# Performance work log

Measured on AMD Instinct MI355X. Metric: run time of the kernel, lower is better.

## Reference

```python
import jax, jax.numpy as jnp
import numpy as np

K_NEIGHBOURS = 16
ITERATIONS = 3
NUM_CLASSES = 20
N_POINTS = 20000


def setup_inputs() -> dict:
    key = jax.random.key(0)
    k1, k2 = jax.random.split(key)
    logits = jax.random.normal(k1, (N_POINTS, NUM_CLASSES), dtype=jnp.float32)
    coords = jax.random.uniform(k2, (N_POINTS, 3), dtype=jnp.float32)
    # nn.init.eye_ then *= -0.1
    compat_w = (-0.1 * jnp.eye(NUM_CLASSES, dtype=jnp.float32))
    return {"logits": logits, "coords": coords, "compat_w": compat_w}


def _knn_graph(coords, k):
    # torch.cdist (p=2): euclidean distances, (N, N)
    sq = jnp.sum(coords * coords, axis=-1)
    d2 = sq[:, None] + sq[None, :] - 2.0 * (coords @ coords.T)
    dists = jnp.sqrt(jnp.clip(d2, 0.0))
    # smallest-k -> top_k of negated distances
    _, idx = jax.lax.top_k(-dists, k)  # (N, k)
    return idx


def reference(logits, coords, compat_w):
    knn_idx = _knn_graph(coords, K_NEIGHBOURS)
    q = jax.nn.softmax(logits, axis=-1)
    for _ in range(ITERATIONS):
        neighbour_q = q[knn_idx]            # (N, k, K) gather
        msg = jnp.mean(neighbour_q, axis=1)  # (N, K)
        refined = logits + msg @ compat_w.T  # nn.Linear: x @ W^T
        q = jax.nn.softmax(refined, axis=-1)
    return (refined, q)
```

## Files before the change

### kernel.cpp

```cpp
#include <hip/hip_runtime.h>

#define N_PTS 20000
#define NCLS 20
#define KNN 16
#define GRID 12
#define NCELLS (GRID * GRID * GRID)
#define HCELL (1.0f / (float)GRID)
#define CAND_CAP 640
#define KEY_CAP 128
#define R_TARGET 0.0680f

__device__ __forceinline__ int cell1d(float v) {
    int c = (int)(v * (float)GRID);
    return min(max(c, 0), GRID - 1);
}

__global__ __launch_bounds__(256) void count_scan_kernel(const float* __restrict__ coords,
                                                         int* __restrict__ cellCount,
                                                         int* __restrict__ doneCtr,
                                                         int* __restrict__ cellStart,
                                                         int* __restrict__ cellCursor) {
    const int p = blockIdx.x * blockDim.x + threadIdx.x;
    if (p < N_PTS) {
        const int cx = cell1d(coords[3 * p + 0]);
        const int cy = cell1d(coords[3 * p + 1]);
        const int cz = cell1d(coords[3 * p + 2]);
        atomicAdd(&cellCount[(cz * GRID + cy) * GRID + cx], 1);
    }
    __syncthreads();
    __shared__ bool isLast;
    if (threadIdx.x == 0)
        isLast = (atomicAdd(doneCtr, 1) == (int)gridDim.x - 1);
    __syncthreads();
    if (!isLast) return;

    __shared__ int part[256];
    const int t = threadIdx.x;
    const int base = t * 7;
    int local[7];
    int s = 0;
#pragma unroll
    for (int i = 0; i < 7; ++i) {
        const int c = base + i;
        const int v = (c < NCELLS)
            ? __hip_atomic_load(&cellCount[c], __ATOMIC_RELAXED, __HIP_MEMORY_SCOPE_AGENT)
            : 0;
        local[i] = s;
        s += v;
    }
    part[t] = s;
    __syncthreads();
    for (int off = 1; off < 256; off <<= 1) {
        const int v = part[t] + ((t >= off) ? part[t - off] : 0);
        __syncthreads();
        part[t] = v;
        __syncthreads();
    }
    const int excl = (t > 0) ? part[t - 1] : 0;
#pragma unroll
    for (int i = 0; i < 7; ++i) {
        const int c = base + i;
        if (c < NCELLS) {
            cellStart[c] = excl + local[i];
            cellCursor[c] = excl + local[i];
        }
    }
    if (t == 255) cellStart[NCELLS] = part[255];
}

__global__ __launch_bounds__(256) void scatter_kernel(const float* __restrict__ coords,
                                                      const float* __restrict__ logits,
                                                      int* __restrict__ cellCursor,
                                                      float4* __restrict__ sortedPts,
                                                      int* __restrict__ orig,
                                                      float* __restrict__ ls,
                                                      float* __restrict__ q0s) {
    const int p = blockIdx.x * blockDim.x + threadIdx.x;
    if (p >= N_PTS) return;
    const float x = coords[3 * p + 0];
    const float y = coords[3 * p + 1];
    const float z = coords[3 * p + 2];
    const int c = (cell1d(z) * GRID + cell1d(y)) * GRID + cell1d(x);
    const int pos = atomicAdd(&cellCursor[c], 1);
    sortedPts[pos] = make_float4(x, y, z, __uint_as_float((unsigned)p));
    orig[pos] = p;
    const float4* l4 = (const float4*)(logits + p * NCLS);
    float v[NCLS];
#pragma unroll
    for (int u = 0; u < 5; ++u) {
        const float4 a = l4[u];
        v[4 * u + 0] = a.x; v[4 * u + 1] = a.y;
        v[4 * u + 2] = a.z; v[4 * u + 3] = a.w;
    }
    float4* d4 = (float4*)(ls + pos * NCLS);
#pragma unroll
    for (int u = 0; u < 5; ++u)
        d4[u] = make_float4(v[4 * u], v[4 * u + 1], v[4 * u + 2], v[4 * u + 3]);
    float mx = v[0];
#pragma unroll
    for (int cc = 1; cc < NCLS; ++cc) mx = fmaxf(mx, v[cc]);
    float sum = 0.f;
#pragma unroll
    for (int cc = 0; cc < NCLS; ++cc) { v[cc] = __expf(v[cc] - mx); sum += v[cc]; }
    const float inv = 1.f / sum;
    float4* q4 = (float4*)(q0s + pos * NCLS);
#pragma unroll
    for (int u = 0; u < 5; ++u)
        q4[u] = make_float4(v[4 * u] * inv, v[4 * u + 1] * inv,
                            v[4 * u + 2] * inv, v[4 * u + 3] * inv);
}

__device__ void knn_ladder(const float4* __restrict__ sortedPts,
                           const int* __restrict__ cellStart,
                           const float4 qp, const int s, int hw,
                           unsigned long long* keys, const int lane,
                           int* __restrict__ knn_out) {
    const unsigned long long laneLt = (1ull << lane) - 1ull;
    const int cx = cell1d(qp.x), cy = cell1d(qp.y), cz = cell1d(qp.z);
    float g = 0.9995f * (float)hw * HCELL;
    float tau = g * g;
    int cnt = 0;
    for (int att = 0; att < 16; ++att) {
        cnt = 0;
        const int xlo = max(cx - hw, 0), xhi = min(cx + hw, GRID - 1);
        const int ylo = max(cy - hw, 0), yhi = min(cy + hw, GRID - 1);
        const int zlo = max(cz - hw, 0), zhi = min(cz + hw, GRID - 1);
        for (int zz = zlo; zz <= zhi; ++zz) {
            for (int yy = ylo; yy <= yhi; ++yy) {
                const int rowc = (zz * GRID + yy) * GRID;
                const int beg = cellStart[rowc + xlo];
                const int end = cellStart[rowc + xhi + 1];
                for (int j0 = beg; j0 < end; j0 += 64) {
                    const int j = j0 + lane;
                    const bool jv = j < end;
                    const float4 pt = sortedPts[jv ? j : beg];
                    const float dx = pt.x - qp.x, dy = pt.y - qp.y, dz = pt.z - qp.z;
                    const float d2 = dx * dx + dy * dy + dz * dz;
                    const bool take = jv && (d2 < tau);
                    const unsigned long long mm = __ballot(take);
                    if (take) {
                        const int pos = cnt + (int)__popcll(mm & laneLt);
                        if (pos < KEY_CAP)
                            keys[pos] = (((unsigned long long)__float_as_uint(d2)) << 32) |
                                        (unsigned long long)(unsigned)j;
                    }
                    cnt += (int)__popcll(mm);
                }
            }
        }
        if (cnt >= KNN && cnt <= KEY_CAP) break;
        if (cnt < KNN) {
            if (hw < GRID - 1) { ++hw; g = 0.9995f * (float)hw * HCELL; tau = g * g; }
            else tau *= 2.5f;
        } else {
            tau *= 0.6f;
        }
    }
    const int m = min(cnt, KEY_CAP);
    const unsigned long long k0 = (lane < m) ? keys[lane] : ~0ull;
    const unsigned long long k1 = (lane + 64 < m) ? keys[lane + 64] : ~0ull;
    int r0 = 0, r1 = 0;
    for (int j = 0; j < m; ++j) {
        const unsigned long long kj = keys[j];
        r0 += (kj < k0); r1 += (kj < k1);
    }
    if (lane < m && r0 < KNN)      knn_out[s * KNN + r0] = (int)(unsigned)(k0 & 0xffffffffull);
    if (lane + 64 < m && r1 < KNN) knn_out[s * KNN + r1] = (int)(unsigned)(k1 & 0xffffffffull);
}

__global__ __launch_bounds__(256) void knn_kernel(const float4* __restrict__ sortedPts,
                                                  const int* __restrict__ cellStart,
                                                  int* __restrict__ knn_out) {
    __shared__ float4 cand[CAND_CAP];
    __shared__ unsigned long long keys[4][KEY_CAP];
    const int lane = threadIdx.x & 63;
    const int wave = threadIdx.x >> 6;
    const int c = blockIdx.x;
    const int cz = c / (GRID * GRID);
    const int cy = (c / GRID) % GRID;
    const int cx = c % GRID;
    const int pbeg = cellStart[c];
    const int pend = cellStart[c + 1];
    const int npts = pend - pbeg;
    if (npts <= 0) return;
    const int bd = (cx == 0 || cx == GRID - 1) + (cy == 0 || cy == GRID - 1) +
                   (cz == 0 || cz == GRID - 1);
    const int hs = (bd >= 2) ? 2 : 1;
    const unsigned long long laneLt = (1ull << lane) - 1ull;

    const int xlo = max(cx - hs, 0), xhi = min(cx + hs, GRID - 1);
    const int ylo = max(cy - hs, 0), yhi = min(cy + hs, GRID - 1);
    const int zlo = max(cz - hs, 0), zhi = min(cz + hs, GRID - 1);
    const int ny = yhi - ylo + 1;
    const int nruns = (zhi - zlo + 1) * ny;

    int beg = 0, len = 0;
    if (lane < nruns) {
        const int zz = zlo + lane / ny;
        const int yy = ylo + lane % ny;
        const int rowc = (zz * GRID + yy) * GRID;
        beg = cellStart[rowc + xlo];
        len = cellStart[rowc + xhi + 1] - beg;
    }
    int off = len;
#pragma unroll
    for (int sh = 1; sh < 32; sh <<= 1) {
        const int o = __shfl_up(off, sh, 64);
        if (lane >= sh) off += o;
    }
    const int nc = __shfl(off, nruns - 1);
    off -= len;
    const int ownRun = (cz - zlo) * ny + (cy - ylo);
    const int ownOff = __shfl(off, ownRun) + (pbeg - __shfl(beg, ownRun));

    if (nc <= CAND_CAP) {
        for (int r = wave; r < nruns; r += 4) {
            const int rb = __shfl(beg, r);
            const int rl = __shfl(len, r);
            const int ro = __shfl(off, r);
            for (int i = lane; i < rl; i += 64) {
                float4 pt = sortedPts[rb + i];
                pt.w = __uint_as_float((unsigned)(rb + i));
                cand[ro + i] = pt;
            }
        }
    }
    __syncthreads();

    if (nc > CAND_CAP) {
        for (int idx = wave; idx < npts; idx += 4)
            knn_ladder(sortedPts, cellStart, sortedPts[pbeg + idx], pbeg + idx,
                       hs, keys[wave], lane, knn_out);
        return;
    }

    const float taumaxr = 0.9995f * (float)hs * HCELL;
    const float taumax = taumaxr * taumaxr;

    for (int idx = wave; idx < npts; idx += 4) {
        const int s = pbeg + idx;
        const float4 qp = cand[ownOff + idx];
        float r = R_TARGET;
        const float inv2r = 0.5f / r;
        const float fx = (fminf(qp.x + r, 1.f) - fmaxf(qp.x - r, 0.f)) * inv2r;
        const float fy = (fminf(qp.y + r, 1.f) - fmaxf(qp.y - r, 0.f)) * inv2r;
        const float fz = (fminf(qp.z + r, 1.f) - fmaxf(qp.z - r, 0.f)) * inv2r;
        const float f = fmaxf(fx * fy * fz, 0.05f);
        r = R_TARGET * __powf(f, -0.33333334f);
        float tau = fminf(r * r, taumax);
        bool triedMax = (tau >= taumax * 0.999f);

        int cnt = 0;
        bool ok = false;
        for (int att = 0; att < 5 && !ok; ++att) {
            cnt = 0;
            for (int j0 = 0; j0 < nc; j0 += 64) {
                const int j = j0 + lane;
                float d2 = 1e30f;
                unsigned pw = 0;
                if (j < nc) {
                    const float4 pt = cand[j];
                    const float dx = pt.x - qp.x, dy = pt.y - qp.y, dz = pt.z - qp.z;
                    d2 = dx * dx + dy * dy + dz * dz;
                    pw = __float_as_uint(pt.w);
                }
                const bool take = d2 < tau;
                const unsigned long long mm = __ballot(take);
                if (take) {
                    const int pos = cnt + (int)__popcll(mm & laneLt);
                    if (pos < KEY_CAP)
                        keys[wave][pos] =
                            (((unsigned long long)__float_as_uint(d2)) << 32) |
                            (unsigned long long)pw;
                }
                cnt += (int)__popcll(mm);
            }
            if (cnt >= KNN && cnt <= KEY_CAP) ok = true;
            else if (cnt < KNN) {
                if (triedMax) break;
                tau = taumax; triedMax = true;
            } else tau *= 0.6f;
        }
        if (!ok) {
            knn_ladder(sortedPts, cellStart, qp, s, hs + 1, keys[wave], lane, knn_out);
            continue;
        }
        const int m = cnt;
        const unsigned long long k0 = (lane < m) ? keys[wave][lane] : ~0ull;
        const unsigned long long k1 = (lane + 64 < m) ? keys[wave][lane + 64] : ~0ull;
        int r0 = 0, r1 = 0;
        for (int j = 0; j < m; ++j) {
            const unsigned long long kj = keys[wave][j];
            r0 += (kj < k0); r1 += (kj < k1);
        }
        if (lane < m && r0 < KNN)      knn_out[s * KNN + r0] = (int)(unsigned)(k0 & 0xffffffffull);
        if (lane + 64 < m && r1 < KNN) knn_out[s * KNN + r1] = (int)(unsigned)(k1 & 0xffffffffull);
    }
}

__global__ __launch_bounds__(256) void crf_iter_kernel(const float* __restrict__ ls,
                                                       const float* __restrict__ W,
                                                       const int* __restrict__ knn,
                                                       const float* __restrict__ qin,
                                                       float* __restrict__ qout,
                                                       const int* __restrict__ orig,
                                                       float* __restrict__ outRef,
                                                       float* __restrict__ outQ) {
    __shared__ float Ws[NCLS * NCLS];
    for (int i = threadIdx.x; i < NCLS * NCLS; i += blockDim.x) Ws[i] = W[i];
    __syncthreads();
    const int t = blockIdx.x * blockDim.x + threadIdx.x;
    const int p = t >> 3;
    const int sub = t & 7;
    if (p >= N_PTS) return;

    float acc[NCLS];
#pragma unroll
    for (int c = 0; c < NCLS; ++c) acc[c] = 0.f;

    const int2 k2 = ((const int2*)(knn + p * KNN))[sub];
    const int ids[2] = {k2.x, k2.y};
#pragma unroll
    for (int u = 0; u < 2; ++u) {
        unsigned id = (unsigned)ids[u];
        if (id >= N_PTS) id = 0;
        const float4* r4 = (const float4*)(qin + id * NCLS);
#pragma unroll
        for (int v = 0; v < 5; ++v) {
            const float4 a = r4[v];
            acc[4 * v + 0] += a.x; acc[4 * v + 1] += a.y;
            acc[4 * v + 2] += a.z; acc[4 * v + 3] += a.w;
        }
    }
#pragma unroll
    for (int c = 0; c < NCLS; ++c) {
        acc[c] += __shfl_xor(acc[c], 1, 64);
        acc[c] += __shfl_xor(acc[c], 2, 64);
        acc[c] += __shfl_xor(acc[c], 4, 64);
        acc[c] *= (1.f / 16.f);
    }

    const int c0 = (sub & 3) * 5;
    float ref[5];
#pragma unroll
    for (int i = 0; i < 5; ++i) {
        float s = ls[p * NCLS + c0 + i];
#pragma unroll
        for (int k = 0; k < NCLS; ++k) s += acc[k] * Ws[(c0 + i) * NCLS + k];
        ref[i] = s;
    }

    float mx = ref[0];
#pragma unroll
    for (int i = 1; i < 5; ++i) mx = fmaxf(mx, ref[i]);
    mx = fmaxf(mx, __shfl_xor(mx, 1, 64));
    mx = fmaxf(mx, __shfl_xor(mx, 2, 64));
    float ex[5];
    float ps = 0.f;
#pragma unroll
    for (int i = 0; i < 5; ++i) { ex[i] = __expf(ref[i] - mx); ps += ex[i]; }
    ps += __shfl_xor(ps, 1, 64);
    ps += __shfl_xor(ps, 2, 64);
    const float inv = 1.f / ps;

    if (sub < 4) {
        if (outRef != nullptr) {
            const int o = orig[p];
#pragma unroll
            for (int i = 0; i < 5; ++i) {
                outRef[o * NCLS + c0 + i] = ref[i];
                outQ[o * NCLS + c0 + i] = ex[i] * inv;
            }
        } else {
#pragma unroll
            for (int i = 0; i < 5; ++i) qout[p * NCLS + c0 + i] = ex[i] * inv;
        }
    }
}

extern "C" void kernel_launch(void* const* d_in, const int* in_sizes, int n_in,
                              void* d_out, int out_size, void* d_ws, size_t ws_size,
                              hipStream_t stream) {
    const float* logits = (const float*)d_in[0];
    const float* coords = (const float*)d_in[1];
    const float* W      = (const float*)d_in[2];
    float* out = (float*)d_out;

    char* ws = (char*)d_ws;
    size_t off = 0;
    int* knn = (int*)(ws + off);              off += (size_t)N_PTS * KNN * 4;
    off = (off + 255) & ~(size_t)255;
    float* ls = (float*)(ws + off);           off += (size_t)N_PTS * NCLS * 4;
    off = (off + 255) & ~(size_t)255;
    float* q0s = (float*)(ws + off);          off += (size_t)N_PTS * NCLS * 4;
    off = (off + 255) & ~(size_t)255;
    float4* sortedPts = (float4*)(ws + off);  off += (size_t)N_PTS * 16;
    off = (off + 255) & ~(size_t)255;
    int* orig = (int*)(ws + off);             off += (size_t)N_PTS * 4;
    off = (off + 255) & ~(size_t)255;
    int* cellCount = (int*)(ws + off);        off += (size_t)(NCELLS + 1) * 4;
    int* doneCtr   = cellCount + NCELLS;
    off = (off + 255) & ~(size_t)255;
    int* cellStart = (int*)(ws + off);        off += (size_t)(NCELLS + 1) * 4;
    off = (off + 255) & ~(size_t)255;
    int* cellCursor = (int*)(ws + off);
    float* q1s = out + N_PTS * NCLS;

    const int threads = 256;
    const int pblocks = (N_PTS + threads - 1) / threads;
    const int cblocks = (8 * N_PTS + threads - 1) / threads;

    hipMemsetAsync(cellCount, 0, (NCELLS + 1) * sizeof(int), stream);
    count_scan_kernel<<<pblocks, threads, 0, stream>>>(coords, cellCount, doneCtr,
                                                       cellStart, cellCursor);
    scatter_kernel<<<pblocks, threads, 0, stream>>>(coords, logits, cellCursor,
                                                    sortedPts, orig, ls, q0s);
    knn_kernel<<<NCELLS, threads, 0, stream>>>(sortedPts, cellStart, knn);
    crf_iter_kernel<<<cblocks, threads, 0, stream>>>(ls, W, knn, q0s, q1s, orig,
                                                     nullptr, nullptr);
    crf_iter_kernel<<<cblocks, threads, 0, stream>>>(ls, W, knn, q1s, q0s, orig,
                                                     nullptr, nullptr);
    crf_iter_kernel<<<cblocks, threads, 0, stream>>>(ls, W, knn, q0s, nullptr, orig,
                                                     out, out + N_PTS * NCLS);
}
```

Baseline: 126.3 us.

## Fuse first CRF iteration into kNN kernel per grid cell

Merges the kNN search kernel with the first CRF message-passing iteration, so each cell block computes neighbour lists and then immediately gathers softmax probabilities for its own points and writes q1. This removes one kernel launch and lets the block read its just-written knn rows while they are likely still in cache. It also adds a launch_bounds occupancy hint of 8 and a shared copy of the compat matrix. In exchange, blocks with few points underuse lanes in the CRF phase, and register pressure from the fused code may reduce occupancy.

Result: slower. 152.8 us (+21.0%).

```diff
diff --git a/kernel.cpp b/kernel.cpp
--- a/kernel.cpp
+++ b/kernel.cpp
@@ -168,11 +168,16 @@
     if (lane + 64 < m && r1 < KNN) knn_out[s * KNN + r1] = (int)(unsigned)(k1 & 0xffffffffull);
 }
 
-__global__ __launch_bounds__(256) void knn_kernel(const float4* __restrict__ sortedPts,
-                                                  const int* __restrict__ cellStart,
-                                                  int* __restrict__ knn_out) {
+__global__ __launch_bounds__(256, 8) void knn_crf1_kernel(const float4* __restrict__ sortedPts,
+                                                          const int* __restrict__ cellStart,
+                                                          const float* __restrict__ ls,
+                                                          const float* __restrict__ W,
+                                                          const float* __restrict__ q0s,
+                                                          int* __restrict__ knn_out,
+                                                          float* __restrict__ q1s) {
     __shared__ float4 cand[CAND_CAP];
     __shared__ unsigned long long keys[4][KEY_CAP];
+    __shared__ float Ws[NCLS * NCLS];
     const int lane = threadIdx.x & 63;
     const int wave = threadIdx.x >> 6;
     const int c = blockIdx.x;
@@ -183,6 +188,7 @@
     const int pend = cellStart[c + 1];
     const int npts = pend - pbeg;
     if (npts <= 0) return;
+    for (int i = threadIdx.x; i < NCLS * NCLS; i += 256) Ws[i] = W[i];
     const int bd = (cx == 0 || cx == GRID - 1) + (cy == 0 || cy == GRID - 1) +
                    (cz == 0 || cz == GRID - 1);
     const int hs = (bd >= 2) ? 2 : 1;
@@ -231,70 +237,129 @@
         for (int idx = wave; idx < npts; idx += 4)
             knn_ladder(sortedPts, cellStart, sortedPts[pbeg + idx], pbeg + idx,
                        hs, keys[wave], lane, knn_out);
-        return;
-    }
-
-    const float taumaxr = 0.9995f * (float)hs * HCELL;
-    const float taumax = taumaxr * taumaxr;
-
-    for (int idx = wave; idx < npts; idx += 4) {
+    } else {
+        const float taumaxr = 0.9995f * (float)hs * HCELL;
+        const float taumax = taumaxr * taumaxr;
+
+        for (int idx = wave; idx < npts; idx += 4) {
+            const int s = pbeg + idx;
+            const float4 qp = cand[ownOff + idx];
+            float r = R_TARGET;
+            const float inv2r = 0.5f / r;
+            const float fx = (fminf(qp.x + r, 1.f) - fmaxf(qp.x - r, 0.f)) * inv2r;
+            const float fy = (fminf(qp.y + r, 1.f) - fmaxf(qp.y - r, 0.f)) * inv2r;
+            const float fz = (fminf(qp.z + r, 1.f) - fmaxf(qp.z - r, 0.f)) * inv2r;
+            const float f = fmaxf(fx * fy * fz, 0.05f);
+            r = R_TARGET * __powf(f, -0.33333334f);
+            float tau = fminf(r * r, taumax);
+            bool triedMax = (tau >= taumax * 0.999f);
+
+            int cnt = 0;
+            bool ok = false;
+            for (int att = 0; att < 5 && !ok; ++att) {
+                cnt = 0;
+                for (int j0 = 0; j0 < nc; j0 += 64) {
+                    const int j = j0 + lane;
+                    float d2 = 1e30f;
+                    unsigned pw = 0;
+                    if (j < nc) {
+                        const float4 pt = cand[j];
+                        const float dx = pt.x - qp.x, dy = pt.y - qp.y, dz = pt.z - qp.z;
+                        d2 = dx * dx + dy * dy + dz * dz;
+                        pw = __float_as_uint(pt.w);
+                    }
+                    const bool take = d2 < tau;
+                    const unsigned long long mm = __ballot(take);
+                    if (take) {
+                        const int pos = cnt + (int)__popcll(mm & laneLt);
+                        if (pos < KEY_CAP)
+                            keys[wave][pos] =
+                                (((unsigned long long)__float_as_uint(d2)) << 32) |
+                                (unsigned long long)pw;
+                    }
+                    cnt += (int)__popcll(mm);
+                }
+                if (cnt >= KNN && cnt <= KEY_CAP) ok = true;
+                else if (cnt < KNN) {
+                    if (triedMax) break;
+                    tau = taumax; triedMax = true;
+                } else tau *= 0.6f;
+            }
+            if (!ok) {
+                knn_ladder(sortedPts, cellStart, qp, s, hs + 1, keys[wave], lane, knn_out);
+                continue;
+            }
+            const int m = cnt;
+            const unsigned long long k0 = (lane < m) ? keys[wave][lane] : ~0ull;
+            const unsigned long long k1 = (lane + 64 < m) ? keys[wave][lane + 64] : ~0ull;
+            int r0 = 0, r1 = 0;
+            for (int j = 0; j < m; ++j) {
+                const unsigned long long kj = keys[wave][j];
+                r0 += (kj < k0); r1 += (kj < k1);
+            }
+            if (lane < m && r0 < KNN)
+                knn_out[s * KNN + r0] = (int)(unsigned)(k0 & 0xffffffffull);
+            if (lane + 64 < m && r1 < KNN)
+                knn_out[s * KNN + r1] = (int)(unsigned)(k1 & 0xffffffffull);
+        }
+    }
+    __syncthreads();
+
+    const int g = lane >> 2;
+    const int sub = lane & 3;
+    const int c0 = sub * 5;
+    for (int idx = wave * 16 + g; idx < npts; idx += 64) {
         const int s = pbeg + idx;
-        const float4 qp = cand[ownOff + idx];
-        float r = R_TARGET;
-        const float inv2r = 0.5f / r;
-        const float fx = (fminf(qp.x + r, 1.f) - fmaxf(qp.x - r, 0.f)) * inv2r;
-        const float fy = (fminf(qp.y + r, 1.f) - fmaxf(qp.y - r, 0.f)) * inv2r;
-        const float fz = (fminf(qp.z + r, 1.f) - fmaxf(qp.z - r, 0.f)) * inv2r;
-        const float f = fmaxf(fx * fy * fz, 0.05f);
-        r = R_TARGET * __powf(f, -0.33333334f);
-        float tau = fminf(r * r, taumax);
-        bool triedMax = (tau >= taumax * 0.999f);
-
-        int cnt = 0;
-        bool ok = false;
-        for (int att = 0; att < 5 && !ok; ++att) {
-            cnt = 0;
-            for (int j0 = 0; j0 < nc; j0 += 64) {
-                const int j = j0 + lane;
-                float d2 = 1e30f;
-                unsigned pw = 0;
-                if (j < nc) {
-                    const float4 pt = cand[j];
-                    const float dx = pt.x - qp.x, dy = pt.y - qp.y, dz = pt.z - qp.z;
-                    d2 = dx * dx + dy * dy + dz * dz;
-                    pw = __float_as_uint(pt.w);
+        const int4 k4 = ((const int4*)(knn_out + s * KNN))[sub];
+        float ref[5];
+#pragma unroll
+        for (int i = 0; i < 5; ++i) ref[i] = ls[s * NCLS + c0 + i];
+#pragma unroll
+        for (int half = 0; half < 2; ++half) {
+            float acc[10];
+#pragma unroll
+            for (int i = 0; i < 10; ++i) acc[i] = 0.f;
+            const int ids[4] = {k4.x, k4.y, k4.z, k4.w};
+#pragma unroll
+            for (int u = 0; u < 4; ++u) {
+                unsigned id = (unsigned)ids[u];
+                if (id >= N_PTS) id = 0;
+                const float2* r2 = (const float2*)(q0s + id * NCLS) + half * 5;
+#pragma unroll
+                for (int v = 0; v < 5; ++v) {
+                    const float2 a = r2[v];
+                    acc[2 * v + 0] += a.x;
+                    acc[2 * v + 1] += a.y;
                 }
-                const bool take = d2 < tau;
-                const unsigned long long mm = __ballot(take);
-                if (take) {
-                    const int pos = cnt + (int)__popcll(mm & laneLt);
-                    if (pos < KEY_CAP)
-                        keys[wave][pos] =
-                            (((unsigned long long)__float_as_uint(d2)) << 32) |
-                            (unsigned long long)pw;
-                }
-                cnt += (int)__popcll(mm);
-            }
-            if (cnt >= KNN && cnt <= KEY_CAP) ok = true;
-            else if (cnt < KNN) {
-                if (triedMax) break;
-                tau = taumax; triedMax = true;
-            } else tau *= 0.6f;
-        }
-        if (!ok) {
-            knn_ladder(sortedPts, cellStart, qp, s, hs + 1, keys[wave], lane, knn_out);
-            continue;
-        }
-        const int m = cnt;
-        const unsigned long long k0 = (lane < m) ? keys[wave][lane] : ~0ull;
-        const unsigned long long k1 = (lane + 64 < m) ? keys[wave][lane + 64] : ~0ull;
-        int r0 = 0, r1 = 0;
-        for (int j = 0; j < m; ++j) {
-            const unsigned long long kj = keys[wave][j];
-            r0 += (kj < k0); r1 += (kj < k1);
-        }
-        if (lane < m && r0 < KNN)      knn_out[s * KNN + r0] = (int)(unsigned)(k0 & 0xffffffffull);
-        if (lane + 64 < m && r1 < KNN) knn_out[s * KNN + r1] = (int)(unsigned)(k1 & 0xffffffffull);
+            }
+#pragma unroll
+            for (int k = 0; k < 10; ++k) {
+                acc[k] += __shfl_xor(acc[k], 1, 64);
+                acc[k] += __shfl_xor(acc[k], 2, 64);
+            }
+#pragma unroll
+            for (int i = 0; i < 5; ++i) {
+                float sv = 0.f;
+#pragma unroll
+                for (int k = 0; k < 10; ++k)
+                    sv += acc[k] * Ws[(c0 + i) * NCLS + half * 10 + k];
+                ref[i] += sv * (1.f / 16.f);
+            }
+        }
+        float mx = ref[0];
+#pragma unroll
+        for (int i = 1; i < 5; ++i) mx = fmaxf(mx, ref[i]);
+        mx = fmaxf(mx, __shfl_xor(mx, 1, 64));
+        mx = fmaxf(mx, __shfl_xor(mx, 2, 64));
+        float ex[5];
+        float ps = 0.f;
+#pragma unroll
+        for (int i = 0; i < 5; ++i) { ex[i] = __expf(ref[i] - mx); ps += ex[i]; }
+        ps += __shfl_xor(ps, 1, 64);
+        ps += __shfl_xor(ps, 2, 64);
+        const float inv = 1.f / ps;
+#pragma unroll
+        for (int i = 0; i < 5; ++i) q1s[s * NCLS + c0 + i] = ex[i] * inv;
     }
 }
 
@@ -415,9 +480,8 @@
                                                        cellStart, cellCursor);
     scatter_kernel<<<pblocks, threads, 0, stream>>>(coords, logits, cellCursor,
                                                     sortedPts, orig, ls, q0s);
-    knn_kernel<<<NCELLS, threads, 0, stream>>>(sortedPts, cellStart, knn);
-    crf_iter_kernel<<<cblocks, threads, 0, stream>>>(ls, W, knn, q0s, q1s, orig,
-                                                     nullptr, nullptr);
+    knn_crf1_kernel<<<NCELLS, threads, 0, stream>>>(sortedPts, cellStart, ls, W,
+                                                    q0s, knn, q1s);
     crf_iter_kernel<<<cblocks, threads, 0, stream>>>(ls, W, knn, q1s, q0s, orig,
                                                      nullptr, nullptr);
     crf_iter_kernel<<<cblocks, threads, 0, stream>>>(ls, W, knn, q0s, nullptr, orig,
```

## Fuse count/scan and scatter into one kernel with a spin-wait ready flag

Applied to the files above, without the earlier changes.

Merges the counting/prefix-scan kernel and the scatter kernel into a single build kernel. The last block to finish counting performs the scan and sets a global ready flag, while every block spins on that flag before scattering. This removes one kernel launch and the boundary between the two stages, and reuses coordinates already held in registers. In exchange it relies on all 79 blocks being co-resident, which they are on this GPU; otherwise the spin-wait could deadlock.

New measurement: 125.0 us. No clear change (-1.0%).

```diff
diff --git a/kernel.cpp b/kernel.cpp
--- a/kernel.cpp
+++ b/kernel.cpp
@@ -15,72 +15,79 @@
     return min(max(c, 0), GRID - 1);
 }
 
-__global__ __launch_bounds__(256) void count_scan_kernel(const float* __restrict__ coords,
-                                                         int* __restrict__ cellCount,
-                                                         int* __restrict__ doneCtr,
-                                                         int* __restrict__ cellStart,
-                                                         int* __restrict__ cellCursor) {
+__global__ __launch_bounds__(256) void build_kernel(const float* __restrict__ coords,
+                                                    const float* __restrict__ logits,
+                                                    int* __restrict__ cellCount,
+                                                    int* __restrict__ doneCtr,
+                                                    int* __restrict__ readyFlag,
+                                                    int* __restrict__ cellStart,
+                                                    int* __restrict__ cellCursor,
+                                                    float4* __restrict__ sortedPts,
+                                                    int* __restrict__ orig,
+                                                    float* __restrict__ ls,
+                                                    float* __restrict__ q0s) {
     const int p = blockIdx.x * blockDim.x + threadIdx.x;
-    if (p < N_PTS) {
-        const int cx = cell1d(coords[3 * p + 0]);
-        const int cy = cell1d(coords[3 * p + 1]);
-        const int cz = cell1d(coords[3 * p + 2]);
-        atomicAdd(&cellCount[(cz * GRID + cy) * GRID + cx], 1);
+    const bool act = (p < N_PTS);
+    float x = 0.f, y = 0.f, z = 0.f;
+    int c = 0;
+    if (act) {
+        x = coords[3 * p + 0];
+        y = coords[3 * p + 1];
+        z = coords[3 * p + 2];
+        c = (cell1d(z) * GRID + cell1d(y)) * GRID + cell1d(x);
+        atomicAdd(&cellCount[c], 1);
     }
     __syncthreads();
     __shared__ bool isLast;
     if (threadIdx.x == 0)
         isLast = (atomicAdd(doneCtr, 1) == (int)gridDim.x - 1);
     __syncthreads();
-    if (!isLast) return;
-
-    __shared__ int part[256];
-    const int t = threadIdx.x;
-    const int base = t * 7;
-    int local[7];
-    int s = 0;
-#pragma unroll
-    for (int i = 0; i < 7; ++i) {
-        const int c = base + i;
-        const int v = (c < NCELLS)
-            ? __hip_atomic_load(&cellCount[c], __ATOMIC_RELAXED, __HIP_MEMORY_SCOPE_AGENT)
-            : 0;
-        local[i] = s;
-        s += v;
-    }
-    part[t] = s;
+
+    if (isLast) {
+        __shared__ int part[256];
+        const int t = threadIdx.x;
+        const int base = t * 7;
+        int local[7];
+        int s = 0;
+#pragma unroll
+        for (int i = 0; i < 7; ++i) {
+            const int cc = base + i;
+            const int v = (cc < NCELLS)
+                ? __hip_atomic_load(&cellCount[cc], __ATOMIC_RELAXED, __HIP_MEMORY_SCOPE_AGENT)
+                : 0;
+            local[i] = s;
+            s += v;
+        }
+        part[t] = s;
+        __syncthreads();
+        for (int off2 = 1; off2 < 256; off2 <<= 1) {
+            const int v = part[t] + ((t >= off2) ? part[t - off2] : 0);
+            __syncthreads();
+            part[t] = v;
+            __syncthreads();
+        }
+        const int excl = (t > 0) ? part[t - 1] : 0;
+#pragma unroll
+        for (int i = 0; i < 7; ++i) {
+            const int cc = base + i;
+            if (cc < NCELLS) {
+                cellStart[cc] = excl + local[i];
+                __hip_atomic_store(&cellCursor[cc], excl + local[i],
+                                   __ATOMIC_RELAXED, __HIP_MEMORY_SCOPE_AGENT);
+            }
+        }
+        if (t == 255) cellStart[NCELLS] = part[255];
+        __syncthreads();
+        if (t == 0)
+            __hip_atomic_store(readyFlag, 1, __ATOMIC_RELAXED, __HIP_MEMORY_SCOPE_AGENT);
+    }
+    if (threadIdx.x == 0) {
+        while (__hip_atomic_load(readyFlag, __ATOMIC_RELAXED, __HIP_MEMORY_SCOPE_AGENT) == 0)
+            __builtin_amdgcn_s_sleep(2);
+    }
     __syncthreads();
-    for (int off = 1; off < 256; off <<= 1) {
-        const int v = part[t] + ((t >= off) ? part[t - off] : 0);
-        __syncthreads();
-        part[t] = v;
-        __syncthreads();
-    }
-    const int excl = (t > 0) ? part[t - 1] : 0;
-#pragma unroll
-    for (int i = 0; i < 7; ++i) {
-        const int c = base + i;
-        if (c < NCELLS) {
-            cellStart[c] = excl + local[i];
-            cellCursor[c] = excl + local[i];
-        }
-    }
-    if (t == 255) cellStart[NCELLS] = part[255];
-}
-
-__global__ __launch_bounds__(256) void scatter_kernel(const float* __restrict__ coords,
-                                                      const float* __restrict__ logits,
-                                                      int* __restrict__ cellCursor,
-                                                      float4* __restrict__ sortedPts,
-                                                      int* __restrict__ orig,
-                                                      float* __restrict__ ls,
-                                                      float* __restrict__ q0s) {
-    const int p = blockIdx.x * blockDim.x + threadIdx.x;
-    if (p >= N_PTS) return;
-    const float x = coords[3 * p + 0];
-    const float y = coords[3 * p + 1];
-    const float z = coords[3 * p + 2];
-    const int c = (cell1d(z) * GRID + cell1d(y)) * GRID + cell1d(x);
+    if (!act) return;
+
     const int pos = atomicAdd(&cellCursor[c], 1);
     sortedPts[pos] = make_float4(x, y, z, __uint_as_float((unsigned)p));
     orig[pos] = p;
@@ -98,10 +105,10 @@
         d4[u] = make_float4(v[4 * u], v[4 * u + 1], v[4 * u + 2], v[4 * u + 3]);
     float mx = v[0];
 #pragma unroll
-    for (int cc = 1; cc < NCLS; ++cc) mx = fmaxf(mx, v[cc]);
+    for (int cc2 = 1; cc2 < NCLS; ++cc2) mx = fmaxf(mx, v[cc2]);
     float sum = 0.f;
 #pragma unroll
-    for (int cc = 0; cc < NCLS; ++cc) { v[cc] = __expf(v[cc] - mx); sum += v[cc]; }
+    for (int cc2 = 0; cc2 < NCLS; ++cc2) { v[cc2] = __expf(v[cc2] - mx); sum += v[cc2]; }
     const float inv = 1.f / sum;
     float4* q4 = (float4*)(q0s + pos * NCLS);
 #pragma unroll
@@ -398,8 +405,9 @@
     off = (off + 255) & ~(size_t)255;
     int* orig = (int*)(ws + off);             off += (size_t)N_PTS * 4;
     off = (off + 255) & ~(size_t)255;
-    int* cellCount = (int*)(ws + off);        off += (size_t)(NCELLS + 1) * 4;
+    int* cellCount = (int*)(ws + off);        off += (size_t)(NCELLS + 2) * 4;
     int* doneCtr   = cellCount + NCELLS;
+    int* readyFlag = cellCount + NCELLS + 1;
     off = (off + 255) & ~(size_t)255;
     int* cellStart = (int*)(ws + off);        off += (size_t)(NCELLS + 1) * 4;
     off = (off + 255) & ~(size_t)255;
@@ -410,11 +418,10 @@
     const int pblocks = (N_PTS + threads - 1) / threads;
     const int cblocks = (8 * N_PTS + threads - 1) / threads;
 
-    hipMemsetAsync(cellCount, 0, (NCELLS + 1) * sizeof(int), stream);
-    count_scan_kernel<<<pblocks, threads, 0, stream>>>(coords, cellCount, doneCtr,
-                                                       cellStart, cellCursor);
-    scatter_kernel<<<pblocks, threads, 0, stream>>>(coords, logits, cellCursor,
-                                                    sortedPts, orig, ls, q0s);
+    hipMemsetAsync(cellCount, 0, (NCELLS + 2) * sizeof(int), stream);
+    build_kernel<<<pblocks, threads, 0, stream>>>(coords, logits, cellCount, doneCtr,
+                                                  readyFlag, cellStart, cellCursor,
+                                                  sortedPts, orig, ls, q0s);
     knn_kernel<<<NCELLS, threads, 0, stream>>>(sortedPts, cellStart, knn);
     crf_iter_kernel<<<cblocks, threads, 0, stream>>>(ls, W, knn, q0s, q1s, orig,
                                                      nullptr, nullptr);
```
